# Optimization experiments

Hardware: AMD Instinct MI355X
Metric: run time of the kernel (lower is better)

## Reference

```python
import jax, jax.numpy as jnp
import numpy as np

F, N, D, K = 32, 4096, 64, 512
COMMITMENT_COST = 0.25


def setup_inputs() -> dict:
    key = jax.random.key(0)
    k1, k2 = jax.random.split(key)
    inputs = jax.random.normal(k1, (F, N, D), dtype=jnp.float32)
    # GlorotUniform on weight shape [F, D, K]
    limit = float(np.sqrt(6.0 / (D + K)))
    w = jax.random.uniform(k2, (F, D, K), dtype=jnp.float32, minval=-limit, maxval=limit)
    return {"inputs": inputs, "w": w}


def reference(inputs, w):
    # inputs: [F, N, D], w: [F, D, K]
    distances = (
        jnp.sum(inputs ** 2, axis=2, keepdims=True)
        - 2.0 * jnp.einsum('fnd,fdk->fnk', inputs, w)
        + jnp.sum(w ** 2, axis=1, keepdims=True)
    )
    enc_idx = jnp.argmin(distances, axis=2)  # [F, N]
    w_t = jnp.swapaxes(w, 1, 2)  # [F, K, D]
    quantized = jnp.take_along_axis(w_t, enc_idx[:, :, None], axis=1)  # [F, N, D]
    e_latent_loss = jnp.mean((jax.lax.stop_gradient(quantized) - inputs) ** 2)
    q_latent_loss = jnp.mean((quantized - jax.lax.stop_gradient(inputs)) ** 2)
    loss = q_latent_loss + COMMITMENT_COST * e_latent_loss
    # straight-through estimator
    output = inputs + jax.lax.stop_gradient(quantized - inputs)
    return output, loss
```

## Files before the change

kernel.cpp:

```cpp
#include <hip/hip_runtime.h>
#include <math.h>

#define NF 32
#define NN 4096
#define ND 64
#define NK 512

#define LOSS_SCALE (1.25f / (float)(NF * NN * ND))
#define TAU 3e-4f

#define NPARTIAL (NF * NN * 4 / 256)

typedef short bf16x8 __attribute__((ext_vector_type(8)));
typedef float f32x4 __attribute__((ext_vector_type(4)));

static __device__ __forceinline__ unsigned short f2bf_rne(float f) {
    unsigned int u = __float_as_uint(f);
    u += 0x7FFFu + ((u >> 16) & 1u);
    return (unsigned short)(u >> 16);
}
static __device__ __forceinline__ float bf2f(unsigned short h) {
    return __uint_as_float(((unsigned int)h) << 16);
}

static __device__ __forceinline__ void gload_lds16(const void* g, void* l) {
    __builtin_amdgcn_global_load_lds(
        (const __attribute__((address_space(1))) unsigned int*)g,
        (__attribute__((address_space(3))) unsigned int*)l, 16, 0, 0);
}

__global__ __launch_bounds__(256)
void vq_prep_w(const float* __restrict__ w, float* __restrict__ wt,
               unsigned short* __restrict__ wh, unsigned short* __restrict__ wl,
               float* __restrict__ w2h) {
    const int gid = blockIdx.x * 256 + threadIdx.x;
    const int dc = gid & 7;
    const int k  = (gid >> 3) & (NK - 1);
    const int f  = gid >> 12;
    const float* __restrict__ wf = w + (size_t)f * ND * NK;
    const size_t rowo = ((size_t)f * NK + k) * ND + dc * 8;

    float v[8];
    unsigned short hh[8], ll[8];
    float s = 0.0f;
#pragma unroll
    for (int j = 0; j < 8; ++j) {
        v[j] = wf[(dc * 8 + j) * NK + k];
        s = fmaf(v[j], v[j], s);
        hh[j] = f2bf_rne(v[j]);
        ll[j] = f2bf_rne(v[j] - bf2f(hh[j]));
    }
    *(float4*)(wt + rowo)     = make_float4(v[0], v[1], v[2], v[3]);
    *(float4*)(wt + rowo + 4) = make_float4(v[4], v[5], v[6], v[7]);
    *(ushort4*)(wh + rowo)     = make_ushort4(hh[0], hh[1], hh[2], hh[3]);
    *(ushort4*)(wh + rowo + 4) = make_ushort4(hh[4], hh[5], hh[6], hh[7]);
    *(ushort4*)(wl + rowo)     = make_ushort4(ll[0], ll[1], ll[2], ll[3]);
    *(ushort4*)(wl + rowo + 4) = make_ushort4(ll[4], ll[5], ll[6], ll[7]);

    s += __shfl_xor(s, 1, 64);
    s += __shfl_xor(s, 2, 64);
    s += __shfl_xor(s, 4, 64);
    if (dc == 0) w2h[f * NK + k] = 0.5f * s;
}

__global__ __launch_bounds__(256, 4)
void vq_argmin(const float* __restrict__ x_in,
               const unsigned short* __restrict__ wh,
               const unsigned short* __restrict__ wl,
               const float* __restrict__ w2h,
               unsigned int* __restrict__ keys,
               unsigned char* __restrict__ flags) {
    const int b    = blockIdx.x;
    const int j    = b >> 3;
    const int f    = (b & 7) * 4 + (j & 3);
    const int xt   = j >> 2;
    const int tid  = threadIdx.x;
    const int wave = tid >> 6;
    const int lane = tid & 63;
    const int lc   = lane & 15;
    const int q    = lane >> 4;
    const int n0   = xt * 128 + wave * 32;

    __shared__ float w2s[NK];
    __shared__ __align__(16) unsigned short bstage[2][4096];

    for (int t = tid; t < NK; t += 256) w2s[t] = w2h[f * NK + t];

    bf16x8 ah[2][2], al[2][2];
    const float* __restrict__ xbase = x_in + ((size_t)f * NN + n0 + lc) * ND;
#pragma unroll
    for (int mt = 0; mt < 2; ++mt) {
#pragma unroll
        for (int s = 0; s < 2; ++s) {
            const float* p = xbase + mt * 16 * ND + s * 32 + q * 8;
            float4 u0 = *(const float4*)(p);
            float4 u1 = *(const float4*)(p + 4);
            float xv[8] = {-u0.x, -u0.y, -u0.z, -u0.w, -u1.x, -u1.y, -u1.z, -u1.w};
            bf16x8 h, l;
#pragma unroll
            for (int jj = 0; jj < 8; ++jj) {
                unsigned short hb = f2bf_rne(xv[jj]);
                unsigned short lb = f2bf_rne(xv[jj] - bf2f(hb));
                h[jj] = (short)hb;
                l[jj] = (short)lb;
            }
            ah[mt][s] = h;
            al[mt][s] = l;
        }
    }

    const unsigned short* __restrict__ whf = wh + (size_t)f * NK * ND;
    const unsigned short* __restrict__ wlf = wl + (size_t)f * NK * ND;

    float m1[8], m2[8], kmin[8];
#pragma unroll
    for (int ri = 0; ri < 8; ++ri) { m1[ri] = INFINITY; m2[ri] = INFINITY; kmin[ri] = INFINITY; }

#define STAGE(st, pb) do {                                                  \
    _Pragma("unroll")                                                       \
    for (int rep = 0; rep < 2; ++rep) {                                     \
        const int c  = wave * 2 + rep;                                      \
        const int tl = c >> 2;                                              \
        const int sg = (c >> 1) & 1;                                        \
        const unsigned short* src = ((c & 1) ? wlf : whf) +                 \
            (size_t)((st) * 32 + tl * 16 + lc) * ND + q * 8 + sg * 32;      \
        gload_lds16(src, &bstage[pb][c * 512]);                             \
    }                                                                       \
} while (0)

    STAGE(0, 0);

    for (int st = 0; st < 16; ++st) {
        __syncthreads();
        if (st < 15) STAGE(st + 1, (st + 1) & 1);
        const unsigned short* __restrict__ bb = &bstage[st & 1][0];

#pragma unroll
        for (int tl = 0; tl < 2; ++tl) {
            const int col = st * 32 + tl * 16 + lc;
            bf16x8 bh0 = *(const bf16x8*)(bb + (tl * 4 + 0) * 512 + lane * 8);
            bf16x8 bl0 = *(const bf16x8*)(bb + (tl * 4 + 1) * 512 + lane * 8);
            bf16x8 bh1 = *(const bf16x8*)(bb + (tl * 4 + 2) * 512 + lane * 8);
            bf16x8 bl1 = *(const bf16x8*)(bb + (tl * 4 + 3) * 512 + lane * 8);
            const float w2 = w2s[col];
#pragma unroll
            for (int mt = 0; mt < 2; ++mt) {
                f32x4 c = {w2, w2, w2, w2};
                c = __builtin_amdgcn_mfma_f32_16x16x32_bf16(ah[mt][0], bh0, c, 0, 0, 0);
                c = __builtin_amdgcn_mfma_f32_16x16x32_bf16(ah[mt][1], bh1, c, 0, 0, 0);
                c = __builtin_amdgcn_mfma_f32_16x16x32_bf16(ah[mt][0], bl0, c, 0, 0, 0);
                c = __builtin_amdgcn_mfma_f32_16x16x32_bf16(ah[mt][1], bl1, c, 0, 0, 0);
                c = __builtin_amdgcn_mfma_f32_16x16x32_bf16(al[mt][0], bh0, c, 0, 0, 0);
                c = __builtin_amdgcn_mfma_f32_16x16x32_bf16(al[mt][1], bh1, c, 0, 0, 0);
                c = __builtin_amdgcn_mfma_f32_16x16x32_bf16(al[mt][0], bl0, c, 0, 0, 0);
                c = __builtin_amdgcn_mfma_f32_16x16x32_bf16(al[mt][1], bl1, c, 0, 0, 0);
#pragma unroll
                for (int r = 0; r < 4; ++r) {
                    const int ri = mt * 4 + r;
                    const float sc = c[r];
                    const float key = __uint_as_float(
                        (__float_as_uint(sc) & 0xFFFFFE00u) | (unsigned int)col);
                    kmin[ri] = fminf(kmin[ri], key);
                    m2[ri] = __builtin_amdgcn_fmed3f(sc, m1[ri], m2[ri]);
                    m1[ri] = fminf(sc, m1[ri]);
                }
            }
        }
    }

#pragma unroll
    for (int ri = 0; ri < 8; ++ri) {
        float a1 = m1[ri], a2 = m2[ri], ak = kmin[ri];
#pragma unroll
        for (int off = 1; off < 16; off <<= 1) {
            const float b1 = __shfl_xor(a1, off, 64);
            const float b2 = __shfl_xor(a2, off, 64);
            const float bk = __shfl_xor(ak, off, 64);
            a2 = fminf(fminf(a2, b2), fmaxf(a1, b1));
            a1 = fminf(a1, b1);
            ak = fminf(ak, bk);
        }
        m1[ri] = a1; m2[ri] = a2; kmin[ri] = ak;
    }

    if (lc == 0) {
#pragma unroll
        for (int mt = 0; mt < 2; ++mt) {
            const int g = f * NN + n0 + mt * 16 + q * 4;
            uint4 kv;
            uchar4 fl;
#pragma unroll
            for (int r = 0; r < 4; ++r) {
                const int ri = mt * 4 + r;
                ((unsigned int*)&kv)[r] = __float_as_uint(kmin[ri]) & 0x1FFu;
                ((unsigned char*)&fl)[r] = (m2[ri] - m1[ri] < TAU) ? 1 : 0;
            }
            *(uint4*)(keys + g) = kv;
            *(uchar4*)(flags + g) = fl;
        }
    }
}

__global__ __launch_bounds__(256)
void vq_rescue(const float* __restrict__ x_in, const float* __restrict__ wt,
               const float* __restrict__ w2h,
               const unsigned char* __restrict__ flags,
               unsigned int* __restrict__ keys) {
    const int lane = threadIdx.x & 63;
    const int wid  = (blockIdx.x * 256 + threadIdx.x) >> 6;
    const int base = wid * 16;

    const unsigned char flv = flags[base + (lane & 15)];
    unsigned long long m = __ballot(flv != 0 && lane < 16);
    while (m) {
        const int r = __ffsll(m) - 1;
        m &= m - 1;
        const int g = base + r;
        const int f = g >> 12;
        const float* __restrict__ xr  = x_in + (size_t)g * ND;
        const float* __restrict__ wtf = wt + (size_t)f * NK * ND;
        unsigned long long best = 0xFFFFFFFFFFFFFFFFULL;
#pragma unroll 1
        for (int jj = 0; jj < 8; ++jj) {
            const int col = jj * 64 + lane;
            const float* __restrict__ wr = wtf + (size_t)col * ND;
            float t = w2h[f * NK + col];
#pragma unroll
            for (int d = 0; d < ND; d += 4) {
                float4 xv = *(const float4*)(xr + d);
                float4 wv = *(const float4*)(wr + d);
                t = fmaf(-xv.x, wv.x, t);
                t = fmaf(-xv.y, wv.y, t);
                t = fmaf(-xv.z, wv.z, t);
                t = fmaf(-xv.w, wv.w, t);
            }
            unsigned int u = __float_as_uint(t);
            u ^= (unsigned int)((int)u >> 31) | 0x80000000u;
            const unsigned long long key =
                ((unsigned long long)u << 32) | (unsigned int)col;
            best = key < best ? key : best;
        }
#pragma unroll
        for (int off = 32; off > 0; off >>= 1) {
            const unsigned long long o = __shfl_xor(best, off, 64);
            best = o < best ? o : best;
        }
        if (lane == 0) keys[g] = (unsigned int)(best & 0xFFFFFFFFULL);
    }
}

__global__ __launch_bounds__(256)
void vq_gather(const float* __restrict__ x_in, const float* __restrict__ wt,
               const unsigned int* __restrict__ keys, float* __restrict__ out,
               float* __restrict__ partial) {
    const int gid = blockIdx.x * 256 + threadIdx.x;
    const int row = gid >> 2;
    const int c   = (gid & 3) * 16;
    const int f   = row >> 12;
    const unsigned int k = keys[row];

    const float* __restrict__ q16 = wt + ((size_t)f * NK + k) * ND + c;
    const float* __restrict__ x16 = x_in + (size_t)row * ND + c;
    float* __restrict__ o16       = out + (size_t)row * ND + c;

    float lsum = 0.0f;
#pragma unroll
    for (int jj = 0; jj < 4; ++jj) {
        float4 qv = *(const float4*)(q16 + 4 * jj);
        float4 xv = *(const float4*)(x16 + 4 * jj);
        const float dx0 = qv.x - xv.x;
        const float dx1 = qv.y - xv.y;
        const float dx2 = qv.z - xv.z;
        const float dx3 = qv.w - xv.w;
        lsum = fmaf(dx0, dx0, lsum);
        lsum = fmaf(dx1, dx1, lsum);
        lsum = fmaf(dx2, dx2, lsum);
        lsum = fmaf(dx3, dx3, lsum);
        *(float4*)(o16 + 4 * jj) = qv;
    }

#pragma unroll
    for (int off = 32; off > 0; off >>= 1) {
        lsum += __shfl_down(lsum, off, 64);
    }
    __shared__ float wsum[4];
    if ((threadIdx.x & 63) == 0) wsum[threadIdx.x >> 6] = lsum;
    __syncthreads();
    if (threadIdx.x == 0) {
        partial[blockIdx.x] = wsum[0] + wsum[1] + wsum[2] + wsum[3];
    }
}

__global__ __launch_bounds__(256)
void vq_loss_final(const float* __restrict__ partial, float* __restrict__ loss) {
    float s = 0.0f;
    for (int i = threadIdx.x; i < NPARTIAL; i += 256) s += partial[i];
#pragma unroll
    for (int off = 32; off > 0; off >>= 1) s += __shfl_down(s, off, 64);
    __shared__ float wsum[4];
    if ((threadIdx.x & 63) == 0) wsum[threadIdx.x >> 6] = s;
    __syncthreads();
    if (threadIdx.x == 0) {
        *loss = (wsum[0] + wsum[1] + wsum[2] + wsum[3]) * LOSS_SCALE;
    }
}

extern "C" void kernel_launch(void* const* d_in, const int* in_sizes, int n_in,
                              void* d_out, int out_size, void* d_ws, size_t ws_size,
                              hipStream_t stream) {
    const float* x_in = (const float*)d_in[0];
    const float* w    = (const float*)d_in[1];
    float* out        = (float*)d_out;

    float* wt  = (float*)d_ws;
    float* w2h = wt + (size_t)NF * NK * ND;
    unsigned short* wh = (unsigned short*)(w2h + NF * NK);
    unsigned short* wl = wh + (size_t)NF * NK * ND;
    unsigned int* keys = (unsigned int*)(wl + (size_t)NF * NK * ND);
    unsigned char* flags = (unsigned char*)(keys + (size_t)NF * NN);
    float* partial = (float*)(flags + (size_t)NF * NN);

    float* loss_slot = out + (size_t)NF * NN * ND;

    vq_prep_w<<<NF * NK * 8 / 256, 256, 0, stream>>>(w, wt, wh, wl, w2h);

    vq_argmin<<<NF * NN / 128, 256, 0, stream>>>(x_in, wh, wl, w2h, keys, flags);

    vq_rescue<<<NF * NN / 16 / 4, 256, 0, stream>>>(x_in, wt, w2h, flags, keys);

    vq_gather<<<NF * NN * 4 / 256, 256, 0, stream>>>(x_in, wt, keys, out, partial);

    vq_loss_final<<<1, 256, 0, stream>>>(partial, loss_slot);
}
```

Before: 165.4 us.

## Split codebook across wave pairs and drop low-low bf16 MFMA terms

```diff
diff --git a/kernel.cpp b/kernel.cpp
--- a/kernel.cpp
+++ b/kernel.cpp
@@ -63,7 +63,7 @@
     if (dc == 0) w2h[f * NK + k] = 0.5f * s;
 }
 
-__global__ __launch_bounds__(256, 4)
+__global__ __launch_bounds__(512, 8)
 void vq_argmin(const float* __restrict__ x_in,
                const unsigned short* __restrict__ wh,
                const unsigned short* __restrict__ wl,
@@ -79,12 +79,15 @@
     const int lane = tid & 63;
     const int lc   = lane & 15;
     const int q    = lane >> 4;
-    const int n0   = xt * 128 + wave * 32;
+    const int h    = wave & 1;
+    const int rg   = wave >> 1;
+    const int n0   = xt * 128 + rg * 32;
 
     __shared__ float w2s[NK];
-    __shared__ __align__(16) unsigned short bstage[2][4096];
-
-    for (int t = tid; t < NK; t += 256) w2s[t] = w2h[f * NK + t];
+    __shared__ __align__(16) unsigned short bstage[2][2][4096];
+    __shared__ float smrg[3][2][128];
+
+    w2s[tid & (NK - 1)] = w2h[f * NK + (tid & (NK - 1))];
 
     bf16x8 ah[2][2], al[2][2];
     const float* __restrict__ xbase = x_in + ((size_t)f * NN + n0 + lc) * ND;
@@ -96,16 +99,16 @@
             float4 u0 = *(const float4*)(p);
             float4 u1 = *(const float4*)(p + 4);
             float xv[8] = {-u0.x, -u0.y, -u0.z, -u0.w, -u1.x, -u1.y, -u1.z, -u1.w};
-            bf16x8 h, l;
+            bf16x8 hh, ll;
 #pragma unroll
             for (int jj = 0; jj < 8; ++jj) {
                 unsigned short hb = f2bf_rne(xv[jj]);
                 unsigned short lb = f2bf_rne(xv[jj] - bf2f(hb));
-                h[jj] = (short)hb;
-                l[jj] = (short)lb;
+                hh[jj] = (short)hb;
+                ll[jj] = (short)lb;
             }
-            ah[mt][s] = h;
-            al[mt][s] = l;
+            ah[mt][s] = hh;
+            al[mt][s] = ll;
         }
     }
 
@@ -116,28 +119,31 @@
 #pragma unroll
     for (int ri = 0; ri < 8; ++ri) { m1[ri] = INFINITY; m2[ri] = INFINITY; kmin[ri] = INFINITY; }
 
-#define STAGE(st, pb) do {                                                  \
+#define STAGE(i_, pb) do {                                                  \
     _Pragma("unroll")                                                       \
     for (int rep = 0; rep < 2; ++rep) {                                     \
         const int c  = wave * 2 + rep;                                      \
-        const int tl = c >> 2;                                              \
-        const int sg = (c >> 1) & 1;                                        \
-        const unsigned short* src = ((c & 1) ? wlf : whf) +                 \
-            (size_t)((st) * 32 + tl * 16 + lc) * ND + q * 8 + sg * 32;      \
-        gload_lds16(src, &bstage[pb][c * 512]);                             \
+        const int ch = c >> 3;                                              \
+        const int r  = c & 7;                                               \
+        const int tl = r >> 2;                                              \
+        const int sg = (r >> 1) & 1;                                        \
+        const int sti = ch * 8 + (i_);                                      \
+        const unsigned short* src = ((r & 1) ? wlf : whf) +                 \
+            (size_t)(sti * 32 + tl * 16 + lc) * ND + q * 8 + sg * 32;       \
+        gload_lds16(src, &bstage[pb][ch][r * 512]);                         \
     }                                                                       \
 } while (0)
 
     STAGE(0, 0);
 
-    for (int st = 0; st < 16; ++st) {
+    for (int i = 0; i < 8; ++i) {
         __syncthreads();
-        if (st < 15) STAGE(st + 1, (st + 1) & 1);
-        const unsigned short* __restrict__ bb = &bstage[st & 1][0];
+        if (i < 7) STAGE(i + 1, (i + 1) & 1);
+        const unsigned short* __restrict__ bb = &bstage[i & 1][h][0];
 
 #pragma unroll
         for (int tl = 0; tl < 2; ++tl) {
-            const int col = st * 32 + tl * 16 + lc;
+            const int col = (h * 8 + i) * 32 + tl * 16 + lc;
             bf16x8 bh0 = *(const bf16x8*)(bb + (tl * 4 + 0) * 512 + lane * 8);
             bf16x8 bl0 = *(const bf16x8*)(bb + (tl * 4 + 1) * 512 + lane * 8);
             bf16x8 bh1 = *(const bf16x8*)(bb + (tl * 4 + 2) * 512 + lane * 8);
@@ -152,8 +158,6 @@
                 c = __builtin_amdgcn_mfma_f32_16x16x32_bf16(ah[mt][1], bl1, c, 0, 0, 0);
                 c = __builtin_amdgcn_mfma_f32_16x16x32_bf16(al[mt][0], bh0, c, 0, 0, 0);
                 c = __builtin_amdgcn_mfma_f32_16x16x32_bf16(al[mt][1], bh1, c, 0, 0, 0);
-                c = __builtin_amdgcn_mfma_f32_16x16x32_bf16(al[mt][0], bl0, c, 0, 0, 0);
-                c = __builtin_amdgcn_mfma_f32_16x16x32_bf16(al[mt][1], bl1, c, 0, 0, 0);
 #pragma unroll
                 for (int r = 0; r < 4; ++r) {
                     const int ri = mt * 4 + r;
@@ -186,18 +190,28 @@
     if (lc == 0) {
 #pragma unroll
         for (int mt = 0; mt < 2; ++mt) {
-            const int g = f * NN + n0 + mt * 16 + q * 4;
-            uint4 kv;
-            uchar4 fl;
 #pragma unroll
             for (int r = 0; r < 4; ++r) {
-                const int ri = mt * 4 + r;
-                ((unsigned int*)&kv)[r] = __float_as_uint(kmin[ri]) & 0x1FFu;
-                ((unsigned char*)&fl)[r] = (m2[ri] - m1[ri] < TAU) ? 1 : 0;
+                const int ri  = mt * 4 + r;
+                const int row = rg * 32 + mt * 16 + q * 4 + r;
+                smrg[0][h][row] = m1[ri];
+                smrg[1][h][row] = m2[ri];
+                smrg[2][h][row] = kmin[ri];
             }
-            *(uint4*)(keys + g) = kv;
-            *(uchar4*)(flags + g) = fl;
-        }
+        }
+    }
+    __syncthreads();
+
+    if (tid < 128) {
+        const float a1 = smrg[0][0][tid], b1 = smrg[0][1][tid];
+        const float a2 = smrg[1][0][tid], b2 = smrg[1][1][tid];
+        const float ka = smrg[2][0][tid], kb = smrg[2][1][tid];
+        const float m1f = fminf(a1, b1);
+        const float m2f = fminf(fminf(a2, b2), fmaxf(a1, b1));
+        const float kf  = fminf(ka, kb);
+        const int g = f * NN + xt * 128 + tid;
+        keys[g]  = __float_as_uint(kf) & 0x1FFu;
+        flags[g] = (m2f - m1f < TAU) ? 1 : 0;
     }
 }
 
@@ -324,7 +338,7 @@
 
     vq_prep_w<<<NF * NK * 8 / 256, 256, 0, stream>>>(w, wt, wh, wl, w2h);
 
-    vq_argmin<<<NF * NN / 128, 256, 0, stream>>>(x_in, wh, wl, w2h, keys, flags);
+    vq_argmin<<<NF * NN / 128, 512, 0, stream>>>(x_in, wh, wl, w2h, keys, flags);
 
     vq_rescue<<<NF * NN / 16 / 4, 256, 0, stream>>>(x_in, wt, w2h, flags, keys);
 
```

Result: slower. 402.2 us (+143.1%).

## Split argmin over codebook halves and drop low-low split-bf16 MFMA terms

Applied to the files above, without the earlier changes.

```diff
diff --git a/kernel.cpp b/kernel.cpp
--- a/kernel.cpp
+++ b/kernel.cpp
@@ -68,9 +68,12 @@
                const unsigned short* __restrict__ wh,
                const unsigned short* __restrict__ wl,
                const float* __restrict__ w2h,
-               unsigned int* __restrict__ keys,
-               unsigned char* __restrict__ flags) {
-    const int b    = blockIdx.x;
+               float* __restrict__ pm1,
+               float* __restrict__ pm2,
+               float* __restrict__ pkm) {
+    const int b2   = blockIdx.x;
+    const int h    = b2 & 1;
+    const int b    = b2 >> 1;
     const int j    = b >> 3;
     const int f    = (b & 7) * 4 + (j & 3);
     const int xt   = j >> 2;
@@ -81,10 +84,10 @@
     const int q    = lane >> 4;
     const int n0   = xt * 128 + wave * 32;
 
-    __shared__ float w2s[NK];
+    __shared__ float w2s[256];
     __shared__ __align__(16) unsigned short bstage[2][4096];
 
-    for (int t = tid; t < NK; t += 256) w2s[t] = w2h[f * NK + t];
+    w2s[tid] = w2h[f * NK + h * 256 + tid];
 
     bf16x8 ah[2][2], al[2][2];
     const float* __restrict__ xbase = x_in + ((size_t)f * NN + n0 + lc) * ND;
@@ -96,16 +99,16 @@
             float4 u0 = *(const float4*)(p);
             float4 u1 = *(const float4*)(p + 4);
             float xv[8] = {-u0.x, -u0.y, -u0.z, -u0.w, -u1.x, -u1.y, -u1.z, -u1.w};
-            bf16x8 h, l;
+            bf16x8 hh, ll;
 #pragma unroll
             for (int jj = 0; jj < 8; ++jj) {
                 unsigned short hb = f2bf_rne(xv[jj]);
                 unsigned short lb = f2bf_rne(xv[jj] - bf2f(hb));
-                h[jj] = (short)hb;
-                l[jj] = (short)lb;
+                hh[jj] = (short)hb;
+                ll[jj] = (short)lb;
             }
-            ah[mt][s] = h;
-            al[mt][s] = l;
+            ah[mt][s] = hh;
+            al[mt][s] = ll;
         }
     }
 
@@ -123,26 +126,26 @@
         const int tl = c >> 2;                                              \
         const int sg = (c >> 1) & 1;                                        \
         const unsigned short* src = ((c & 1) ? wlf : whf) +                 \
-            (size_t)((st) * 32 + tl * 16 + lc) * ND + q * 8 + sg * 32;      \
+            (size_t)((h * 8 + (st)) * 32 + tl * 16 + lc) * ND + q * 8 + sg * 32; \
         gload_lds16(src, &bstage[pb][c * 512]);                             \
     }                                                                       \
 } while (0)
 
     STAGE(0, 0);
 
-    for (int st = 0; st < 16; ++st) {
+    for (int st = 0; st < 8; ++st) {
         __syncthreads();
-        if (st < 15) STAGE(st + 1, (st + 1) & 1);
+        if (st < 7) STAGE(st + 1, (st + 1) & 1);
         const unsigned short* __restrict__ bb = &bstage[st & 1][0];
 
 #pragma unroll
         for (int tl = 0; tl < 2; ++tl) {
-            const int col = st * 32 + tl * 16 + lc;
+            const int col = h * 256 + st * 32 + tl * 16 + lc;
             bf16x8 bh0 = *(const bf16x8*)(bb + (tl * 4 + 0) * 512 + lane * 8);
             bf16x8 bl0 = *(const bf16x8*)(bb + (tl * 4 + 1) * 512 + lane * 8);
             bf16x8 bh1 = *(const bf16x8*)(bb + (tl * 4 + 2) * 512 + lane * 8);
             bf16x8 bl1 = *(const bf16x8*)(bb + (tl * 4 + 3) * 512 + lane * 8);
-            const float w2 = w2s[col];
+            const float w2 = w2s[st * 32 + tl * 16 + lc];
 #pragma unroll
             for (int mt = 0; mt < 2; ++mt) {
                 f32x4 c = {w2, w2, w2, w2};
@@ -152,8 +155,6 @@
                 c = __builtin_amdgcn_mfma_f32_16x16x32_bf16(ah[mt][1], bl1, c, 0, 0, 0);
                 c = __builtin_amdgcn_mfma_f32_16x16x32_bf16(al[mt][0], bh0, c, 0, 0, 0);
                 c = __builtin_amdgcn_mfma_f32_16x16x32_bf16(al[mt][1], bh1, c, 0, 0, 0);
-                c = __builtin_amdgcn_mfma_f32_16x16x32_bf16(al[mt][0], bl0, c, 0, 0, 0);
-                c = __builtin_amdgcn_mfma_f32_16x16x32_bf16(al[mt][1], bl1, c, 0, 0, 0);
 #pragma unroll
                 for (int r = 0; r < 4; ++r) {
                     const int ri = mt * 4 + r;
@@ -184,19 +185,16 @@
     }
 
     if (lc == 0) {
+        const size_t FN = (size_t)NF * NN;
 #pragma unroll
         for (int mt = 0; mt < 2; ++mt) {
             const int g = f * NN + n0 + mt * 16 + q * 4;
-            uint4 kv;
-            uchar4 fl;
-#pragma unroll
-            for (int r = 0; r < 4; ++r) {
-                const int ri = mt * 4 + r;
-                ((unsigned int*)&kv)[r] = __float_as_uint(kmin[ri]) & 0x1FFu;
-                ((unsigned char*)&fl)[r] = (m2[ri] - m1[ri] < TAU) ? 1 : 0;
-            }
-            *(uint4*)(keys + g) = kv;
-            *(uchar4*)(flags + g) = fl;
+            float4 v1 = make_float4(m1[mt*4+0], m1[mt*4+1], m1[mt*4+2], m1[mt*4+3]);
+            float4 v2 = make_float4(m2[mt*4+0], m2[mt*4+1], m2[mt*4+2], m2[mt*4+3]);
+            float4 vk = make_float4(kmin[mt*4+0], kmin[mt*4+1], kmin[mt*4+2], kmin[mt*4+3]);
+            *(float4*)(pm1 + h * FN + g) = v1;
+            *(float4*)(pm2 + h * FN + g) = v2;
+            *(float4*)(pkm + h * FN + g) = vk;
         }
     }
 }
@@ -204,14 +202,27 @@
 __global__ __launch_bounds__(256)
 void vq_rescue(const float* __restrict__ x_in, const float* __restrict__ wt,
                const float* __restrict__ w2h,
-               const unsigned char* __restrict__ flags,
+               const float* __restrict__ pm1, const float* __restrict__ pm2,
+               const float* __restrict__ pkm,
                unsigned int* __restrict__ keys) {
     const int lane = threadIdx.x & 63;
     const int wid  = (blockIdx.x * 256 + threadIdx.x) >> 6;
     const int base = wid * 16;
-
-    const unsigned char flv = flags[base + (lane & 15)];
-    unsigned long long m = __ballot(flv != 0 && lane < 16);
+    const size_t FN = (size_t)NF * NN;
+
+    int flag = 0;
+    if (lane < 16) {
+        const int g = base + lane;
+        const float a1 = pm1[g], b1 = pm1[FN + g];
+        const float a2 = pm2[g], b2 = pm2[FN + g];
+        const float ka = pkm[g], kb = pkm[FN + g];
+        const float m1f = fminf(a1, b1);
+        const float m2f = fminf(fminf(a2, b2), fmaxf(a1, b1));
+        const float kf  = fminf(ka, kb);
+        keys[g] = __float_as_uint(kf) & 0x1FFu;
+        flag = (m2f - m1f < TAU) ? 1 : 0;
+    }
+    unsigned long long m = __ballot(flag != 0);
     while (m) {
         const int r = __ffsll(m) - 1;
         m &= m - 1;
@@ -317,16 +328,18 @@
     unsigned short* wh = (unsigned short*)(w2h + NF * NK);
     unsigned short* wl = wh + (size_t)NF * NK * ND;
     unsigned int* keys = (unsigned int*)(wl + (size_t)NF * NK * ND);
-    unsigned char* flags = (unsigned char*)(keys + (size_t)NF * NN);
-    float* partial = (float*)(flags + (size_t)NF * NN);
+    float* pm1 = (float*)(keys + (size_t)NF * NN);
+    float* pm2 = pm1 + (size_t)2 * NF * NN;
+    float* pkm = pm2 + (size_t)2 * NF * NN;
+    float* partial = pkm + (size_t)2 * NF * NN;
 
     float* loss_slot = out + (size_t)NF * NN * ND;
 
     vq_prep_w<<<NF * NK * 8 / 256, 256, 0, stream>>>(w, wt, wh, wl, w2h);
 
-    vq_argmin<<<NF * NN / 128, 256, 0, stream>>>(x_in, wh, wl, w2h, keys, flags);
-
-    vq_rescue<<<NF * NN / 16 / 4, 256, 0, stream>>>(x_in, wt, w2h, flags, keys);
+    vq_argmin<<<NF * NN / 64, 256, 0, stream>>>(x_in, wh, wl, w2h, pm1, pm2, pkm);
+
+    vq_rescue<<<NF * NN / 16 / 4, 256, 0, stream>>>(x_in, wt, w2h, pm1, pm2, pkm, keys);
 
     vq_gather<<<NF * NN * 4 / 256, 256, 0, stream>>>(x_in, wt, keys, out, partial);
 
```

Measured after the change: 165.8 us. Within noise of the previous version (+0.2%).
